# Kernel tuning notes

Hardware: AMD Instinct MI355X
Metric: run time of the kernel (lower is better)

The kernel has to match this reference:

```python
import jax, jax.numpy as jnp
import numpy as np

# Fixed production-scale dims (see shape_source)
B, R, WIDTH, T, H, W = 8, 12, 2304, 4, 16, 29
REDUCE, HID, NC, ROI_SP, DEPTH = 1024, 512, 60, 7, 2
SR = 2  # roi_align sampling ratio (fixed; torchvision default -1 is roi-adaptive)


def conv2d(x, w, pad):
    return jax.lax.conv_general_dilated(
        x, w, (1, 1), [(pad, pad), (pad, pad)],
        dimension_numbers=('NCHW', 'OIHW', 'NCHW'))


def maxpool_3x3_s2(x):
    return jax.lax.reduce_window(
        x, -jnp.inf, jax.lax.max, (1, 1, 3, 3), (1, 1, 2, 2),
        [(0, 0), (0, 0), (1, 1), (1, 1)])


def bilinear(img, ys, xs):
    # img [C,h,w]; ys, xs [P] -> [C,P]; matches torchvision bilinear_interpolate
    h, w = img.shape[1], img.shape[2]
    valid = (ys >= -1.0) & (ys <= h) & (xs >= -1.0) & (xs <= w)
    y = jnp.clip(ys, 0.0, h - 1.0)
    x = jnp.clip(xs, 0.0, w - 1.0)
    y0f = jnp.floor(y); x0f = jnp.floor(x)
    iy0 = y0f.astype(jnp.int32); ix0 = x0f.astype(jnp.int32)
    iy1 = jnp.minimum(iy0 + 1, h - 1); ix1 = jnp.minimum(ix0 + 1, w - 1)
    ly = y - y0f; lx = x - x0f; hy = 1.0 - ly; hx = 1.0 - lx
    v00 = img[:, iy0, ix0]; v01 = img[:, iy0, ix1]
    v10 = img[:, iy1, ix0]; v11 = img[:, iy1, ix1]
    out = hy * hx * v00 + hy * lx * v01 + ly * hx * v10 + ly * lx * v11
    return jnp.where(valid[None, :], out, 0.0)


def roi_align_one(img, box):
    # img [C,H,W]; box (x1,y1,x2,y2) in feature coords; aligned=False, scale=1
    x1, y1, x2, y2 = box[0], box[1], box[2], box[3]
    rw = jnp.maximum(x2 - x1, 1.0)
    rh = jnp.maximum(y2 - y1, 1.0)
    bw = rw / ROI_SP; bh = rh / ROI_SP
    g = (jnp.arange(ROI_SP, dtype=jnp.float32)[:, None]
         + (jnp.arange(SR, dtype=jnp.float32)[None, :] + 0.5) / SR).reshape(-1)  # [7*SR]
    ys = y1 + g * bh; xs = x1 + g * bw
    n = ROI_SP * SR
    yy = jnp.repeat(ys, n); xx = jnp.tile(xs, n)
    vals = bilinear(img, yy, xx)                       # [C, n*n]
    vals = vals.reshape(img.shape[0], ROI_SP, SR, ROI_SP, SR)
    return vals.mean(axis=(2, 4))                      # [C,7,7]


def hr2o_layer(x, qw, kw, vw, cw, gamma, beta):
    # x [R, HID, Hp, Wp]; non-local attention across ROIs of one image
    q = conv2d(x, qw, 1)
    k = conv2d(x, kw, 1)
    v = conv2d(x, vw, 1)
    att = jnp.einsum('ichw,jchw->ijhw', q, k) / jnp.sqrt(jnp.float32(HID))
    att = jax.nn.softmax(att, axis=1)                  # softmax over key rois
    virt = jnp.einsum('ijhw,jchw->ichw', att, v)
    mu = virt.mean(axis=(1, 2, 3), keepdims=True)      # GroupNorm(1, HID)
    var = virt.var(axis=(1, 2, 3), keepdims=True)
    virt = (virt - mu) / jnp.sqrt(var + 1e-5)
    virt = virt * gamma[None, :, None, None] + beta[None, :, None, None]
    virt = jax.nn.relu(virt)
    virt = conv2d(virt, cw, 1)                         # mlp_1x1=False -> 3x3 pad 1
    return x + virt                                    # dropout inactive in eval


def setup_inputs() -> dict:
    key = jax.random.key(0)
    ks = jax.random.split(key, 14)
    features = jax.random.normal(ks[0], (B, WIDTH, T, H, W), jnp.float32)
    xy = jax.random.uniform(ks[1], (B, R, 2), minval=0.0, maxval=0.6)
    wh = jax.random.uniform(ks[2], (B, R, 2), minval=0.2, maxval=0.4)
    rois = jnp.concatenate([xy, xy + wh], axis=-1)     # normalized x1,y1,x2,y2

    def w_(k, shape, fan_in):
        return jax.random.normal(k, shape, jnp.float32) * (1.0 / np.sqrt(fan_in))

    return {
        'features': features,
        'rois': rois,
        'conv_reduce_w': w_(ks[3], (REDUCE, WIDTH, 1, 1), WIDTH),
        'conv1_w': w_(ks[4], (HID, 2 * REDUCE, 1, 1), 2 * REDUCE),
        'conv2_w': w_(ks[5], (HID, HID, 3, 3), HID * 9),
        'hr2o_qw': w_(ks[6], (DEPTH, HID, HID, 3, 3), HID * 9),
        'hr2o_kw': w_(ks[7], (DEPTH, HID, HID, 3, 3), HID * 9),
        'hr2o_vw': w_(ks[8], (DEPTH, HID, HID, 3, 3), HID * 9),
        'hr2o_cw': w_(ks[9], (DEPTH, HID, HID, 3, 3), HID * 9),
        'hr2o_gamma': jnp.ones((DEPTH, HID), jnp.float32),
        'hr2o_beta': jnp.zeros((DEPTH, HID), jnp.float32),
        'fc1_w': w_(ks[10], (HID, REDUCE), REDUCE),
        'fc2_w': w_(ks[11], (NC, 2 * HID), 2 * HID),
    }


def reference(features, rois, conv_reduce_w, conv1_w, conv2_w,
              hr2o_qw, hr2o_kw, hr2o_vw, hr2o_cw, hr2o_gamma, hr2o_beta,
              fc1_w, fc2_w):
    feats = features.mean(axis=2)                      # AdaptiveAvgPool3d((1,H,W)) over T
    feats = conv2d(feats, conv_reduce_w, 0)            # [B, REDUCE, H, W]

    scale = jnp.array([W, H, W, H], jnp.float32)
    boxes = rois * scale                               # feature-space coords (detached)
    ra = jax.vmap(lambda img, bxs: jax.vmap(lambda b: roi_align_one(img, b))(bxs))(
        feats, boxes)                                  # [B, R, REDUCE, 7, 7]
    roi_feats = ra.max(axis=(-2, -1)).reshape(B * R, REDUCE)  # MaxPool2d(7)

    # broadcast bg + tiled actor, concat on channels (eff_h=H, eff_w=W)
    bg = jnp.broadcast_to(feats[:, None], (B, R, REDUCE, H, W))
    actor = jnp.broadcast_to(
        roi_feats.reshape(B, R, REDUCE)[..., None, None], (B, R, REDUCE, H, W))
    x = jnp.concatenate([bg, actor], axis=2).reshape(B * R, 2 * REDUCE, H, W)
    x = jax.nn.relu(conv2d(x, conv1_w, 0))             # 1x1
    x = jax.nn.relu(conv2d(x, conv2_w, 0))             # 3x3, Conv2d default pad=0
    x = maxpool_3x3_s2(x)                              # [B*R, HID, 7, 14]
    hp, wp = x.shape[2], x.shape[3]
    x = x.reshape(B, R, HID, hp, wp)
    for d in range(DEPTH):
        x = jax.vmap(lambda xi: hr2o_layer(
            xi, hr2o_qw[d], hr2o_kw[d], hr2o_vw[d], hr2o_cw[d],
            hr2o_gamma[d], hr2o_beta[d]))(x)
    high = x.mean(axis=(-2, -1)).reshape(B * R, HID)   # GAP

    out = jax.nn.relu(roi_feats @ fc1_w.T)
    out = jnp.concatenate([out, high], axis=1)
    return out @ fc2_w.T                               # [B*R, NC]
```

## Files before the change

kernel.cpp:

```cpp
#include <hip/hip_runtime.h>
#include <math.h>

#define BB 8
#define RR 12
#define WIDTH 2304
#define TT 4
#define HH 16
#define WW 29
#define HWIN (HH*WW)
#define REDUCE 1024
#define HID 512
#define NC 60
#define DEPTH 2
#define NIMG (BB*RR)
#define OH2 14
#define OW2 27
#define NSP2 (OH2*OW2)
#define PH 7
#define PW 14
#define NSP (PH*PW)
#define ATT_SCALE 0.044194173824159216f

typedef __attribute__((ext_vector_type(8))) short short8;
typedef __attribute__((ext_vector_type(4))) float floatx4;

__device__ __forceinline__ void split2(float v, unsigned short& h, unsigned short& l)
{
    union { float f; unsigned u; } c; c.f = v;
    unsigned hb = c.u & 0xffff0000u;
    h = (unsigned short)(hb >> 16);
    union { float f; unsigned u; } hc; hc.u = hb;
    float r = v - hc.f;
    union { float f; unsigned u; } rc; rc.f = r;
    unsigned ru = rc.u + 0x7fffu + ((rc.u >> 16) & 1u);
    l = (unsigned short)(ru >> 16);
}

__device__ __forceinline__ void gll16(const void* g, void* l)
{
    __builtin_amdgcn_global_load_lds((const __attribute__((address_space(1))) void*)g,
                                     (__attribute__((address_space(3))) void*)l,
                                     16, 0, 0);
}

#define MFMA3(d, ah_, al_, bh_, bl_) \
    d = __builtin_amdgcn_mfma_f32_16x16x32_bf16(ah_, bh_, d, 0, 0, 0); \
    d = __builtin_amdgcn_mfma_f32_16x16x32_bf16(ah_, bl_, d, 0, 0, 0); \
    d = __builtin_amdgcn_mfma_f32_16x16x32_bf16(al_, bh_, d, 0, 0, 0);

template<int TYPE, int NSEL, bool RELU, bool RESID, int KW, int KSTN, int MTOT, long PLSTR, int NREAL, bool ZX>
__global__ __launch_bounds__(256, 2)
void tap2_k(const int4* __restrict__ WA0, const int4* __restrict__ WA1, const int4* __restrict__ WA2,
            const ushort* __restrict__ BH, const ushort* __restrict__ BL,
            const float* __restrict__ Res,
            float* __restrict__ Y0, float* __restrict__ Y1, float* __restrict__ Y2)
{
    __shared__ int4 L[3872];
    const int tid = threadIdx.x;
    const int z  = ZX ? blockIdx.x : blockIdx.z;
    const int nb = ZX ? blockIdx.z : blockIdx.x;
    int by = blockIdx.y;

    const int4* WA = WA0; float* Y = Y0;
    if (NSEL == 3) {
        int sel = by >> 2; by &= 3;
        if (sel == 1) { WA = WA1; Y = Y1; }
        else if (sel == 2) { WA = WA2; Y = Y2; }
    }
    const int m0 = by * 128;
    const int lane = tid & 63, wv = tid >> 6;
    const int lrow = lane >> 4, lcol = lane & 15;
    constexpr long ALO = (long)KSTN * 4 * MTOT;

    int nU[2], gU[2]; long pbU[2]; bool vU[2];
#pragma unroll
    for (int it = 0; it < 2; ++it) {
        int u = tid + (it << 8);
        vU[it] = (u < 448);
        int uu = vU[it] ? u : 0;
        nU[it] = uu % 112; gU[it] = uu / 112;
        if (TYPE == 0) pbU[it] = nU[it];
        else {
            int gn = nb * 112 + nU[it];
            if (TYPE == 1) pbU[it] = (gn >> 5) * 29 + (gn & 31);
            else pbU[it] = min(gn, NREAL - 1);
        }
    }
    const ushort* BHz = BH + (size_t)z * PLSTR;
    const ushort* BLz = BL + (size_t)z * PLSTR;

    floatx4 acc[2][7];
#pragma unroll
    for (int mf = 0; mf < 2; ++mf)
#pragma unroll
        for (int nf = 0; nf < 7; ++nf) acc[mf][nf] = (floatx4){0.f, 0.f, 0.f, 0.f};

    short8 rbh[2], rbl[2];

#define STAGE_ISSUE(KST, BUF) { \
    int k8 = (KST) * 4; \
    _Pragma("unroll") \
    for (int j = 0; j < 4; ++j) { \
        int h = wv * 4 + j, p = h >> 3, g = (h >> 1) & 3, hf = h & 1; \
        gll16(WA + (p ? ALO : 0) + (long)(k8 + g) * MTOT + m0 + hf * 64 + lane, \
              L + (BUF) * 1936 + (p * 4 + g) * 129 + hf * 64); \
    } \
    int tap, ci0, shv; \
    if (TYPE == 2) { tap = 0; ci0 = (KST) << 5; shv = 0; } \
    else { tap = (KST) >> 4; ci0 = ((KST) & 15) << 5; int t3 = tap / 3; \
           shv = (TYPE == 0) ? t3 * 16 + (tap - t3 * 3) : t3 * 29 + (tap - t3 * 3); } \
    _Pragma("unroll") \
    for (int it = 0; it < 2; ++it) if (vU[it]) { \
        size_t o = (size_t)(pbU[it] + shv) * KW + ci0 + gU[it] * 8; \
        rbh[it] = *(const short8*)(BHz + o); \
        rbl[it] = *(const short8*)(BLz + o); \
    } }

#define STAGE_WRITE(BUF) { \
    _Pragma("unroll") \
    for (int it = 0; it < 2; ++it) if (vU[it]) { \
        *((short8*)(L + (BUF) * 1936 + 1032 + gU[it] * 113 + nU[it])) = rbh[it]; \
        *((short8*)(L + (BUF) * 1936 + 1484 + gU[it] * 113 + nU[it])) = rbl[it]; \
    } }

#define COMPUTE(BUF) { \
    const int4* Lc = L + (BUF) * 1936; \
    short8 ah[2], al[2]; \
    _Pragma("unroll") \
    for (int mf = 0; mf < 2; ++mf) { \
        int au = lrow * 129 + (wv * 2 + mf) * 16 + lcol; \
        ah[mf] = *(const short8*)(Lc + au); \
        al[mf] = *(const short8*)(Lc + 516 + au); \
    } \
    _Pragma("unroll") \
    for (int nf = 0; nf < 7; ++nf) { \
        int bu = 1032 + lrow * 113 + nf * 16 + lcol; \
        short8 bh = *(const short8*)(Lc + bu); \
        short8 bl = *(const short8*)(Lc + bu + 452); \
        _Pragma("unroll") \
        for (int mf = 0; mf < 2; ++mf) { MFMA3(acc[mf][nf], ah[mf], al[mf], bh, bl) } \
    } }

    STAGE_ISSUE(0, 0)
    STAGE_WRITE(0)
    __syncthreads();

    int cur = 0;
    for (int kst = 0; kst < KSTN; ++kst) {
        int nxt = cur ^ 1;
        bool more = (kst + 1 < KSTN);
        if (more) STAGE_ISSUE(kst + 1, nxt)
        COMPUTE(cur)
        if (more) { STAGE_WRITE(nxt) __syncthreads(); }
        cur = nxt;
    }

#pragma unroll
    for (int mf = 0; mf < 2; ++mf) {
        int m = m0 + wv * 32 + mf * 16 + lrow * 4;
#pragma unroll
        for (int nf = 0; nf < 7; ++nf) {
            int col = nf * 16 + lcol;
            int sp, realn; bool ok;
            if (TYPE == 0) { int oh = col >> 4, ow = col & 15; ok = ow < 14; sp = oh * 14 + ow; realn = 98; }
            else if (TYPE == 1) { int gn = nb * 112 + col; int oh = gn >> 5, ow = gn & 31; ok = ow < 27; sp = oh * 27 + ow; realn = 378; }
            else { int gn = nb * 112 + col; ok = gn < NREAL; sp = gn; realn = NREAL; }
            if (ok) {
#pragma unroll
                for (int r = 0; r < 4; ++r) {
                    size_t idx = ((size_t)z * MTOT + m + r) * realn + sp;
                    float v = acc[mf][nf][r];
                    if (RESID) v += Res[idx];
                    if (RELU) v = fmaxf(v, 0.f);
                    Y[idx] = v;
                }
            }
        }
    }
#undef STAGE_ISSUE
#undef STAGE_WRITE
#undef COMPUTE
}

__global__ void prep_w_k(const float* __restrict__ s0, const float* __restrict__ s1,
                         const float* __restrict__ s2, const float* __restrict__ s3,
                         int4* __restrict__ dst)
{
    const int c = blockIdx.y;
    const float* src = (c == 0) ? s0 : (c == 1) ? s1 : (c == 2) ? s2 : s3;
    int4* dh = dst + (size_t)c * 589824;
    int4* dl = dh + 294912;
    int idx = blockIdx.x * 256 + threadIdx.x;
    if (idx >= 294912) return;
    int g8 = idx / 512, m = idx & 511;
    unsigned hw[4], lw[4];
#pragma unroll
    for (int j = 0; j < 4; ++j) {
        int k1 = g8 * 8 + 2 * j, k2 = k1 + 1;
        float v1 = src[(size_t)m * 4608 + ((k1 & 511) * 9 + (k1 >> 9))];
        float v2 = src[(size_t)m * 4608 + ((k2 & 511) * 9 + (k2 >> 9))];
        unsigned short h0, l0, h1, l1;
        split2(v1, h0, l0); split2(v2, h1, l1);
        hw[j] = (unsigned)h0 | ((unsigned)h1 << 16);
        lw[j] = (unsigned)l0 | ((unsigned)l1 << 16);
    }
    dh[idx] = make_int4(hw[0], hw[1], hw[2], hw[3]);
    dl[idx] = make_int4(lw[0], lw[1], lw[2], lw[3]);
}

__global__ void prep_wg_k(const float* __restrict__ src, int ldw, int M, int K8,
                          int4* __restrict__ dst)
{
    int idx = blockIdx.x * 256 + threadIdx.x;
    if (idx >= K8 * M) return;
    int g8 = idx / M, m = idx % M;
    unsigned hw[4], lw[4];
#pragma unroll
    for (int j = 0; j < 4; ++j) {
        int k1 = g8 * 8 + 2 * j;
        float v1 = src[(size_t)m * ldw + k1];
        float v2 = src[(size_t)m * ldw + k1 + 1];
        unsigned short h0, l0, h1, l1;
        split2(v1, h0, l0); split2(v2, h1, l1);
        hw[j] = (unsigned)h0 | ((unsigned)h1 << 16);
        lw[j] = (unsigned)l0 | ((unsigned)l1 << 16);
    }
    dst[idx] = make_int4(hw[0], hw[1], hw[2], hw[3]);
    dst[(size_t)K8 * M + idx] = make_int4(lw[0], lw[1], lw[2], lw[3]);
}

__global__ __launch_bounds__(256)
void tsplit_k(const float* __restrict__ src, ushort* __restrict__ dh, ushort* __restrict__ dl,
              int C, int S, long zsrc, long zdst)
{
    __shared__ float t[64][65];
    const int c0 = blockIdx.x * 64, s0 = blockIdx.y * 64, z = blockIdx.z;
    const float* sz = src + (size_t)z * zsrc;
    const int tx = threadIdx.x & 63, ty = threadIdx.x >> 6;
#pragma unroll
    for (int i = 0; i < 16; ++i) {
        int cc = i * 4 + ty;
        int c = c0 + cc, s = s0 + tx;
        t[cc][tx] = (c < C && s < S) ? sz[(size_t)c * S + s] : 0.f;
    }
    __syncthreads();
#pragma unroll
    for (int i = 0; i < 16; ++i) {
        int ss = i * 4 + ty;
        int s = s0 + ss, c = c0 + tx;
        if (s < S && c < C) {
            unsigned short h, l;
            split2(t[tx][ss], h, l);
            size_t o = (size_t)z * zdst + (size_t)s * C + c;
            dh[o] = h; dl[o] = l;
        }
    }
}

__global__ __launch_bounds__(256)
void tsplit_c2_k(const float* __restrict__ bg, const float* __restrict__ bias1,
                 ushort* __restrict__ dh, ushort* __restrict__ dl)
{
    __shared__ float t[64][65];
    const int c0 = blockIdx.x * 64, s0 = blockIdx.y * 64, z = blockIdx.z;
    const int b = z / RR;
    const int tx = threadIdx.x & 63, ty = threadIdx.x >> 6;
#pragma unroll
    for (int i = 0; i < 16; ++i) {
        int cc = i * 4 + ty;
        int s = s0 + tx;
        t[cc][tx] = (s < 464) ? bg[((size_t)b * 512 + c0 + cc) * 464 + s] : 0.f;
    }
    __syncthreads();
    const float bv = bias1[z * 512 + c0 + tx];
#pragma unroll
    for (int i = 0; i < 16; ++i) {
        int ss = i * 4 + ty;
        int s = s0 + ss, c = c0 + tx;
        if (s < 472) {
            float v = (s < 464) ? fmaxf(t[tx][ss] + bv, 0.f) : 0.f;
            unsigned short h, l;
            split2(v, h, l);
            size_t o = (size_t)z * 241664 + (size_t)s * 512 + c;
            dh[o] = h; dl[o] = l;
        }
    }
}

__global__ __launch_bounds__(256)
void tsplit_pad_k(const float* __restrict__ x, ushort* __restrict__ dh, ushort* __restrict__ dl)
{
    __shared__ float t[64 * 99];
    const int c0 = blockIdx.x * 64, z = blockIdx.y;
    const int tid = threadIdx.x;
#pragma unroll
    for (int i = 0; i < 25; ++i) {
        int idx = tid + i * 256;
        if (idx < 6272) {
            int c = idx / 98, s = idx % 98;
            t[c * 99 + s] = x[((size_t)z * 512 + c0 + c) * 98 + s];
        }
    }
    __syncthreads();
#pragma unroll
    for (int i = 0; i < 40; ++i) {
        int idx = tid + i * 256;
        int sp = idx >> 6, c = idx & 63;
        int r = sp >> 4, col = sp & 15;
        float v = (r >= 1 && r <= 7 && col >= 1 && col <= 14) ? t[c * 99 + (r - 1) * 14 + col - 1] : 0.f;
        unsigned short h, l;
        split2(v, h, l);
        size_t o = (size_t)z * 81920 + (size_t)sp * 512 + c0 + c;
        dh[o] = h; dl[o] = l;
    }
}

__global__ void tmean_k(const float* __restrict__ f, float* __restrict__ o, int total)
{
    int i = blockIdx.x * blockDim.x + threadIdx.x;
    if (i >= total) return;
    int p = i % HWIN; long bc = i / HWIN;
    const float* src = f + bc * (long)TT * HWIN + p;
    o[i] = (src[0] + src[HWIN] + src[2 * HWIN] + src[3 * HWIN]) * 0.25f;
}

__global__ __launch_bounds__(256)
void roi_align_k(const float* __restrict__ feats, const float* __restrict__ rois,
                 float* __restrict__ roi_feats)
{
    __shared__ int s_o00[196], s_o01[196], s_o10[196], s_o11[196];
    __shared__ float s_w[4][196];
    const int n = blockIdx.x;
    const int b = n / RR;
    const int t = threadIdx.x;
    if (t < 196) {
        float x1 = rois[n * 4 + 0] * WW, y1 = rois[n * 4 + 1] * HH;
        float x2 = rois[n * 4 + 2] * WW, y2 = rois[n * 4 + 3] * HH;
        float rw = fmaxf(x2 - x1, 1.f), rh = fmaxf(y2 - y1, 1.f);
        float bw = rw / 7.f, bh = rh / 7.f;
        int j = t / 14, i = t % 14;
        float gy = (float)(j >> 1) + ((j & 1) + 0.5f) * 0.5f;
        float gx = (float)(i >> 1) + ((i & 1) + 0.5f) * 0.5f;
        float ys = y1 + gy * bh, xs = x1 + gx * bw;
        bool valid = (ys >= -1.f) && (ys <= (float)HH) && (xs >= -1.f) && (xs <= (float)WW);
        float y = fminf(fmaxf(ys, 0.f), (float)(HH - 1));
        float x = fminf(fmaxf(xs, 0.f), (float)(WW - 1));
        float y0f = floorf(y), x0f = floorf(x);
        int iy0 = (int)y0f, ix0 = (int)x0f;
        int iy1 = min(iy0 + 1, HH - 1), ix1 = min(ix0 + 1, WW - 1);
        float ly = y - y0f, lx = x - x0f, hy = 1.f - ly, hx = 1.f - lx;
        float msk = valid ? 1.f : 0.f;
        s_o00[t] = iy0 * WW + ix0; s_o01[t] = iy0 * WW + ix1;
        s_o10[t] = iy1 * WW + ix0; s_o11[t] = iy1 * WW + ix1;
        s_w[0][t] = hy * hx * msk; s_w[1][t] = hy * lx * msk;
        s_w[2][t] = ly * hx * msk; s_w[3][t] = ly * lx * msk;
    }
    __syncthreads();
    for (int c = t; c < REDUCE; c += 256) {
        const float* img = feats + ((long)(b * REDUCE + c)) * HWIN;
        float mx = -INFINITY;
        for (int bin = 0; bin < 49; ++bin) {
            int by_ = bin / 7, bx = bin % 7;
            float s = 0.f;
#pragma unroll
            for (int sy = 0; sy < 2; ++sy)
#pragma unroll
                for (int sx = 0; sx < 2; ++sx) {
                    int ss = (by_ * 2 + sy) * 14 + bx * 2 + sx;
                    s += s_w[0][ss] * img[s_o00[ss]] + s_w[1][ss] * img[s_o01[ss]]
                       + s_w[2][ss] * img[s_o10[ss]] + s_w[3][ss] * img[s_o11[ss]];
                }
            mx = fmaxf(mx, s * 0.25f);
        }
        roi_feats[(long)n * REDUCE + c] = mx;
    }
}

__global__ void dots_k(const float* __restrict__ Xr, const float* __restrict__ Wt,
                       int ldw, int woff, float* __restrict__ Y,
                       int Nrows, int M, int K, int relu)
{
    int idx = blockIdx.x * blockDim.x + threadIdx.x;
    if (idx >= Nrows * M) return;
    int o = idx / Nrows, n = idx % Nrows;
    const float* xr = Xr + (long)n * K;
    const float* w = Wt + (long)o * ldw + woff;
    float acc = 0.f;
    for (int k = 0; k < K; ++k) acc = fmaf(xr[k], w[k], acc);
    if (relu) acc = fmaxf(acc, 0.f);
    Y[(long)n * M + o] = acc;
}

__global__ void maxpool_k(const float* __restrict__ in, float* __restrict__ out, int total)
{
    int idx = blockIdx.x * blockDim.x + threadIdx.x;
    if (idx >= total) return;
    int ow = idx % PW; int r = idx / PW; int oh = r % PH; long nc = r / PH;
    const float* src = in + nc * NSP2;
    float m = -INFINITY;
    for (int kh = 0; kh < 3; ++kh) {
        int ih = oh * 2 - 1 + kh; if (ih < 0 || ih >= OH2) continue;
        for (int kw = 0; kw < 3; ++kw) {
            int iw = ow * 2 - 1 + kw; if (iw < 0 || iw >= OW2) continue;
            m = fmaxf(m, src[ih * OW2 + iw]);
        }
    }
    out[idx] = m;
}

__global__ __launch_bounds__(256)
void att2_k(const float* __restrict__ q, const float* __restrict__ k, float* __restrict__ att)
{
    __shared__ float qs[5376];
    __shared__ float ks[5376];
    __shared__ float sc[1008];
    const int b = blockIdx.x, p0 = blockIdx.y * 7;
    const int tid = threadIdx.x;

    int itI[4], itJ[4], itP[4]; bool itV[4];
#pragma unroll
    for (int r = 0; r < 4; ++r) {
        int item = tid + (r << 8);
        itV[r] = item < 1008;
        int it = itV[r] ? item : 0;
        int ij = it / 7; itP[r] = it % 7;
        itI[r] = ij / 12; itJ[r] = ij % 12;
    }
    float acc[4] = {0.f, 0.f, 0.f, 0.f};

    for (int cc0 = 0; cc0 < 512; cc0 += 64) {
        for (int l = tid; l < 5376; l += 256) {
            int i = l / 448, r = l % 448, c = r / 7, p = r % 7;
            size_t off = ((size_t)(b * 12 + i) * 512 + cc0 + c) * 98 + p0 + p;
            qs[l] = q[off];
            ks[l] = k[off];
        }
        __syncthreads();
#pragma unroll
        for (int r = 0; r < 4; ++r) {
            if (itV[r]) {
                const float* qp = qs + itI[r] * 448 + itP[r];
                const float* kp = ks + itJ[r] * 448 + itP[r];
                float a = acc[r];
#pragma unroll 8
                for (int c = 0; c < 64; ++c) a = fmaf(qp[c * 7], kp[c * 7], a);
                acc[r] = a;
            }
        }
        __syncthreads();
    }
#pragma unroll
    for (int r = 0; r < 4; ++r)
        if (itV[r]) sc[tid + (r << 8)] = acc[r] * ATT_SCALE;
    __syncthreads();
    if (tid < 84) {
        int i = tid / 7, p = tid % 7;
        float m = -INFINITY;
        float v[12];
#pragma unroll
        for (int j = 0; j < 12; ++j) { v[j] = sc[(i * 12 + j) * 7 + p]; m = fmaxf(m, v[j]); }
        float s = 0.f;
#pragma unroll
        for (int j = 0; j < 12; ++j) { v[j] = expf(v[j] - m); s += v[j]; }
        float inv = 1.f / s;
#pragma unroll
        for (int j = 0; j < 12; ++j)
            att[((size_t)(b * 12 + i) * 12 + j) * 98 + p0 + p] = v[j] * inv;
    }
}

__global__ __launch_bounds__(256)
void virt2_k(const float* __restrict__ att, const float* __restrict__ v, float* __restrict__ virt)
{
    __shared__ float as_[14112];
    const int b = blockIdx.x, cb = blockIdx.y;
    const int tid = threadIdx.x;
    for (int l = tid; l < 14112; l += 256) as_[l] = att[(size_t)b * 14112 + l];
    __syncthreads();

    for (int it = tid; it < 6272; it += 256) {
        int c = cb * 64 + it / 98, p = it % 98;
        float o[12];
#pragma unroll
        for (int i = 0; i < 12; ++i) o[i] = 0.f;
#pragma unroll
        for (int j = 0; j < 12; ++j) {
            float vj = v[((size_t)(b * 12 + j) * 512 + c) * 98 + p];
#pragma unroll
            for (int i = 0; i < 12; ++i) o[i] = fmaf(as_[(i * 12 + j) * 98 + p], vj, o[i]);
        }
#pragma unroll
        for (int i = 0; i < 12; ++i)
            virt[((size_t)(b * 12 + i) * 512 + c) * 98 + p] = o[i];
    }
}

__global__ __launch_bounds__(256)
void stats_k(const float* __restrict__ virt, float* __restrict__ mu, float* __restrict__ rstd)
{
    int n = blockIdx.x;
    const float* src = virt + (long)n * HID * NSP;
    float s = 0.f, q = 0.f;
    for (int i = threadIdx.x; i < HID * NSP; i += 256) {
        float v = src[i]; s += v; q = fmaf(v, v, q);
    }
    for (int off = 32; off; off >>= 1) { s += __shfl_down(s, off); q += __shfl_down(q, off); }
    __shared__ float ss[4], sq[4];
    int w = threadIdx.x >> 6;
    if ((threadIdx.x & 63) == 0) { ss[w] = s; sq[w] = q; }
    __syncthreads();
    if (threadIdx.x == 0) {
        float S = ss[0] + ss[1] + ss[2] + ss[3];
        float Q = sq[0] + sq[1] + sq[2] + sq[3];
        const float invN = 1.f / (HID * NSP);
        float m = S * invN;
        float var = Q * invN - m * m;
        mu[n] = m; rstd[n] = rsqrtf(var + 1e-5f);
    }
}

__global__ void norm_k(float* __restrict__ virt, const float* __restrict__ mu,
                       const float* __restrict__ rstd,
                       const float* __restrict__ gamma, const float* __restrict__ beta)
{
    int idx = blockIdx.x * blockDim.x + threadIdx.x;
    const int TOT = NIMG * HID * NSP;
    if (idx >= TOT) return;
    int n = idx / (HID * NSP);
    int c = (idx / NSP) % HID;
    float val = (virt[idx] - mu[n]) * rstd[n] * gamma[c] + beta[c];
    virt[idx] = fmaxf(val, 0.f);
}

__global__ void meanpool_k(const float* __restrict__ x, float* __restrict__ high)
{
    int idx = blockIdx.x * blockDim.x + threadIdx.x;
    if (idx >= NIMG * HID) return;
    const float* src = x + (long)idx * NSP;
    float s = 0.f;
    for (int p = 0; p < NSP; ++p) s += src[p];
    high[idx] = s * (1.f / NSP);
}

__global__ void final_k(const float* __restrict__ fc1o, const float* __restrict__ high,
                        const float* __restrict__ fc2, float* __restrict__ out)
{
    int idx = blockIdx.x * blockDim.x + threadIdx.x;
    if (idx >= NIMG * NC) return;
    int n = idx / NC, o = idx % NC;
    const float* w = fc2 + (long)o * (2 * HID);
    const float* a = fc1o + (long)n * HID;
    const float* h = high + (long)n * HID;
    float acc = 0.f;
    for (int c = 0; c < HID; ++c) acc = fmaf(a[c], w[c], acc);
    for (int c = 0; c < HID; ++c) acc = fmaf(h[c], w[HID + c], acc);
    out[idx] = acc;
}

extern "C" void kernel_launch(void* const* d_in, const int* in_sizes, int n_in,
                              void* d_out, int out_size, void* d_ws, size_t ws_size,
                              hipStream_t stream)
{
    (void)in_sizes; (void)n_in; (void)out_size; (void)ws_size;
    const float* features = (const float*)d_in[0];
    const float* rois     = (const float*)d_in[1];
    const float* w_reduce = (const float*)d_in[2];
    const float* w_conv1  = (const float*)d_in[3];
    const float* w_conv2  = (const float*)d_in[4];
    const float* qw       = (const float*)d_in[5];
    const float* kw       = (const float*)d_in[6];
    const float* vw       = (const float*)d_in[7];
    const float* cw       = (const float*)d_in[8];
    const float* gamma    = (const float*)d_in[9];
    const float* beta     = (const float*)d_in[10];
    const float* fc1      = (const float*)d_in[11];
    const float* fc2      = (const float*)d_in[12];
    float* ws = (float*)d_ws;

    float*  tmean = ws + 0;
    ushort* tmTH  = (ushort*)(ws + 8552448);
    ushort* tmTL  = (ushort*)(ws + 12828672);
    float*  feats = ws + 17104896;
    ushort* ftTH  = (ushort*)(ws + 0);
    ushort* ftTL  = (ushort*)(ws + 1900544);
    ushort* B2H   = (ushort*)(ws + 0);
    ushort* B2L   = (ushort*)(ws + 11599872);
    int4*   WTQ   = (int4*)(ws + 0);
    float*  bg    = ws + 23199744;
    float*  out2  = ws + 23199744;
    float*  qb    = ws + 23199744;
    float*  kb    = ws + 28016640;
    float*  vb    = ws + 32833536;
    ushort* PTH   = (ushort*)(ws + 41779200);
    ushort* PTL   = (ushort*)(ws + 45711360);
    float*  xb    = ws + 49643520;
    float*  virt  = ws + 54460416;
    int4*   WTS   = (int4*)(ws + 59277312);
    float*  rf    = ws + 61636608;
    float*  bias1 = ws + 61734912;
    float*  fc1o  = ws + 61784064;
    float*  attb  = ws + 61833216;
    float*  mu    = ws + 61946112;
    float*  rstd  = ws + 61946240;
    float*  high  = ws + 61946368;

    dim3 blk(256);

    prep_wg_k<<<1152, blk, 0, stream>>>(w_reduce, 2304, 1024, 288, WTS);

    { int tot = BB * WIDTH * HWIN;
      tmean_k<<<(tot + 255) / 256, blk, 0, stream>>>(features, tmean, tot); }

    tsplit_k<<<dim3(36, 8, 8), blk, 0, stream>>>(tmean, tmTH, tmTL, 2304, 464, 1069056, 1069056);

    tap2_k<2, 1, false, false, 2304, 72, 1024, 464L * 2304, 464, false>
        <<<dim3(5, 8, 8), blk, 0, stream>>>(WTS, nullptr, nullptr, tmTH, tmTL, nullptr,
                                            feats, nullptr, nullptr);

    tsplit_k<<<dim3(16, 8, 8), blk, 0, stream>>>(feats, ftTH, ftTL, 1024, 464, 475136, 475136);

    roi_align_k<<<96, blk, 0, stream>>>(feats, rois, rf);
    dots_k<<<(NIMG * HID + 255) / 256, blk, 0, stream>>>(rf, w_conv1, 2048, 1024, bias1, NIMG, HID, REDUCE, 0);
    dots_k<<<(NIMG * HID + 255) / 256, blk, 0, stream>>>(rf, fc1, 1024, 0, fc1o, NIMG, HID, REDUCE, 1);

    prep_wg_k<<<256, blk, 0, stream>>>(w_conv1, 2048, 512, 128, WTS);
    tap2_k<2, 1, false, false, 1024, 32, 512, 464L * 1024, 464, false>
        <<<dim3(5, 4, 8), blk, 0, stream>>>(WTS, nullptr, nullptr, ftTH, ftTL, nullptr,
                                            bg, nullptr, nullptr);

    prep_w_k<<<dim3(1152, 1), blk, 0, stream>>>(w_conv2, w_conv2, w_conv2, w_conv2, WTS);
    tsplit_c2_k<<<dim3(8, 8, 96), blk, 0, stream>>>(bg, bias1, B2H, B2L);

    tap2_k<1, 1, true, false, 512, 144, 512, 472L * 512, 378, true>
        <<<dim3(96, 4, 4), blk, 0, stream>>>(WTS, nullptr, nullptr, B2H, B2L, nullptr,
                                             out2, nullptr, nullptr);

    { int tot = NIMG * HID * NSP;
      maxpool_k<<<(tot + 255) / 256, blk, 0, stream>>>(out2, xb, tot); }

    for (int d = 0; d < DEPTH; ++d) {
        long woff = (long)d * HID * HID * 9;
        prep_w_k<<<dim3(1152, 4), blk, 0, stream>>>(qw + woff, kw + woff, vw + woff, cw + woff, WTQ);

        tsplit_pad_k<<<dim3(8, 96), blk, 0, stream>>>(xb, PTH, PTL);
        tap2_k<0, 3, false, false, 512, 144, 512, 160L * 512, 98, true>
            <<<dim3(96, 12, 1), blk, 0, stream>>>(WTQ, WTQ + 589824, WTQ + 2 * 589824,
                                                  PTH, PTL, nullptr, qb, kb, vb);

        att2_k<<<dim3(8, 14), blk, 0, stream>>>(qb, kb, attb);
        virt2_k<<<dim3(8, 8), blk, 0, stream>>>(attb, vb, virt);
        stats_k<<<96, blk, 0, stream>>>(virt, mu, rstd);
        { int tot = NIMG * HID * NSP;
          norm_k<<<(tot + 255) / 256, blk, 0, stream>>>(virt, mu, rstd, gamma + d * HID, beta + d * HID); }

        tsplit_pad_k<<<dim3(8, 96), blk, 0, stream>>>(virt, PTH, PTL);
        tap2_k<0, 1, false, true, 512, 144, 512, 160L * 512, 98, true>
            <<<dim3(96, 4, 1), blk, 0, stream>>>(WTQ + 3 * 589824, nullptr, nullptr,
                                                 PTH, PTL, xb, xb, nullptr, nullptr);
    }

    meanpool_k<<<(NIMG * HID + 255) / 256, blk, 0, stream>>>(xb, high);
    final_k<<<(NIMG * NC + 255) / 256, blk, 0, stream>>>(fc1o, high, fc2, (float*)d_out);
}
```

Baseline: 3.314 ms.

## Add larger-tile 3x3 conv GEMM kernel with 512 threads and remapped block order

Adds a new tap3_k kernel for the 3x3 convolutions (conv2, QKV and output convs) that uses 512-thread blocks with 256x224 output tiles. Two images or a wider spatial slab share each weight tile, so weight loads are reused more and per-block overhead drops. The kernel uses a custom block-index swizzle for cache locality and dynamic LDS of about 124KB. The old tap2_k is trimmed to serve only the 1x1 GEMMs. The trade-off is more registers (28 accumulators per thread), fewer blocks, and possibly lower occupancy or a tail effect, e.g. only 96 blocks for the output conv.

```diff
diff --git a/kernel.cpp b/kernel.cpp
--- a/kernel.cpp
+++ b/kernel.cpp
@@ -48,25 +48,172 @@
     d = __builtin_amdgcn_mfma_f32_16x16x32_bf16(ah_, bl_, d, 0, 0, 0); \
     d = __builtin_amdgcn_mfma_f32_16x16x32_bf16(al_, bh_, d, 0, 0, 0);
 
-template<int TYPE, int NSEL, bool RELU, bool RESID, int KW, int KSTN, int MTOT, long PLSTR, int NREAL, bool ZX>
-__global__ __launch_bounds__(256, 2)
-void tap2_k(const int4* __restrict__ WA0, const int4* __restrict__ WA1, const int4* __restrict__ WA2,
+template<int GEOM, int NSEL, bool RELU, bool RESID>
+__global__ __launch_bounds__(512, 2)
+void tap3_k(const int4* __restrict__ WA0, const int4* __restrict__ WA1, const int4* __restrict__ WA2,
             const ushort* __restrict__ BH, const ushort* __restrict__ BL,
             const float* __restrict__ Res,
             float* __restrict__ Y0, float* __restrict__ Y1, float* __restrict__ Y2)
 {
+    extern __shared__ int4 L[];
+    const int tid = threadIdx.x;
+    const int bid = blockIdx.x;
+    int m0, z0, z1 = 0, nb = 0, sel = 0;
+    if (GEOM == 0) {
+        int s = bid & 7, r = bid >> 3;
+        int zq = s & 3, yq = s >> 2;
+        int y = yq * 3 + r % 3;
+        int zp = zq * 12 + r / 3;
+        sel = y >> 1; m0 = (y & 1) * 256;
+        z0 = zp * 2; z1 = z0 + 1;
+    } else if (GEOM == 1) {
+        int s = bid & 7, r = bid >> 3;
+        m0 = (s & 1) * 256;
+        nb = r & 1; z0 = (s >> 1) * 24 + (r >> 1); z1 = z0;
+    } else {
+        int s = bid & 7, r = bid >> 3;
+        m0 = (s & 1) * 256;
+        int zp = (s >> 1) * 12 + r;
+        z0 = zp * 2; z1 = z0 + 1;
+    }
+    const int4* WA = (NSEL == 3) ? (sel == 0 ? WA0 : sel == 1 ? WA1 : WA2) : WA0;
+    float* Y = (NSEL == 3) ? (sel == 0 ? Y0 : sel == 1 ? Y1 : Y2) : Y0;
+
+    const int lane = tid & 63, wv = tid >> 6;
+    const int lrow = lane >> 4, lcol = lane & 15;
+    constexpr long ALO = 294912;
+    constexpr long PLSTR = (GEOM == 1) ? 472L * 512 : 160L * 512;
+
+    const long abase = ((wv >> 2) ? ALO : 0) + m0;
+    const int ag = wv & 3;
+
+    int nU[2], gU[2]; bool vU[2];
+    const ushort* bhp[2]; const ushort* blp[2];
+#pragma unroll
+    for (int it = 0; it < 2; ++it) {
+        int u = tid + (it << 9);
+        vU[it] = (u < 896);
+        int uu = vU[it] ? u : 0;
+        nU[it] = uu % 224; gU[it] = uu / 224;
+        long pb; int zsel;
+        if (GEOM == 1) {
+            int gn = nb * 224 + nU[it];
+            pb = (gn >> 5) * 29 + (gn & 31); zsel = z0;
+        } else {
+            int hi = nU[it] >= 112;
+            pb = nU[it] - (hi ? 112 : 0); zsel = hi ? z1 : z0;
+        }
+        bhp[it] = BH + (size_t)zsel * PLSTR + pb * 512 + gU[it] * 8;
+        blp[it] = BL + (size_t)zsel * PLSTR + pb * 512 + gU[it] * 8;
+    }
+
+    floatx4 acc[2][14];
+#pragma unroll
+    for (int mf = 0; mf < 2; ++mf)
+#pragma unroll
+        for (int nf = 0; nf < 14; ++nf) acc[mf][nf] = (floatx4){0.f, 0.f, 0.f, 0.f};
+
+    short8 rbh[2], rbl[2];
+
+#define STAGE_ISSUE(KST, BUF) { \
+    int k8 = (KST) * 4; \
+    _Pragma("unroll") \
+    for (int j = 0; j < 4; ++j) \
+        gll16(WA + abase + (long)(k8 + ag) * 512 + j * 64 + lane, \
+              L + (BUF) * 2064 + wv * 258 + j * 64); \
+    int tap = (KST) >> 4, ci0 = ((KST) & 15) << 5; \
+    int t3 = tap / 3; \
+    int boff = ((GEOM == 1) ? (t3 * 29 + tap - t3 * 3) : (t3 * 16 + tap - t3 * 3)) * 512 + ci0; \
+    _Pragma("unroll") \
+    for (int it = 0; it < 2; ++it) if (vU[it]) { \
+        rbh[it] = *(const short8*)(bhp[it] + boff); \
+        rbl[it] = *(const short8*)(blp[it] + boff); \
+    } }
+
+#define STAGE_WRITE(BUF) { \
+    _Pragma("unroll") \
+    for (int it = 0; it < 2; ++it) if (vU[it]) { \
+        *((short8*)(L + 4128 + (BUF) * 1800 + gU[it] * 225 + nU[it])) = rbh[it]; \
+        *((short8*)(L + 4128 + (BUF) * 1800 + 900 + gU[it] * 225 + nU[it])) = rbl[it]; \
+    } }
+
+#define COMPUTE(BUF) { \
+    const int4* La = L + (BUF) * 2064; \
+    const int4* Lb = L + 4128 + (BUF) * 1800; \
+    short8 ah[2], al[2]; \
+    _Pragma("unroll") \
+    for (int mf = 0; mf < 2; ++mf) { \
+        int au = lrow * 258 + (wv * 2 + mf) * 16 + lcol; \
+        ah[mf] = *(const short8*)(La + au); \
+        al[mf] = *(const short8*)(La + 1032 + au); \
+    } \
+    _Pragma("unroll") \
+    for (int nf = 0; nf < 14; ++nf) { \
+        int bu = lrow * 225 + nf * 16 + lcol; \
+        short8 bh = *(const short8*)(Lb + bu); \
+        short8 bl = *(const short8*)(Lb + 900 + bu); \
+        _Pragma("unroll") \
+        for (int mf = 0; mf < 2; ++mf) { MFMA3(acc[mf][nf], ah[mf], al[mf], bh, bl) } \
+    } }
+
+    STAGE_ISSUE(0, 0)
+    STAGE_WRITE(0)
+    __syncthreads();
+
+    int cur = 0;
+    for (int kst = 0; kst < 144; ++kst) {
+        int nxt = cur ^ 1;
+        bool more = (kst + 1 < 144);
+        if (more) STAGE_ISSUE(kst + 1, nxt)
+        COMPUTE(cur)
+        if (more) { STAGE_WRITE(nxt) __syncthreads(); }
+        cur = nxt;
+    }
+
+#pragma unroll
+    for (int mf = 0; mf < 2; ++mf) {
+        int m = m0 + wv * 32 + mf * 16 + lrow * 4;
+#pragma unroll
+        for (int nf = 0; nf < 14; ++nf) {
+            int col = nf * 16 + lcol;
+            int sp, realn, z; bool ok;
+            if (GEOM == 1) {
+                int gn = nb * 224 + col;
+                int oh = gn >> 5, ow = gn & 31;
+                ok = ow < 27; sp = oh * 27 + ow; realn = 378; z = z0;
+            } else {
+                int cm = col - (nf >= 7 ? 112 : 0);
+                int oh = cm >> 4, ow = cm & 15;
+                ok = ow < 14; sp = oh * 14 + ow; realn = 98;
+                z = (nf >= 7) ? z1 : z0;
+            }
+            if (ok) {
+#pragma unroll
+                for (int r = 0; r < 4; ++r) {
+                    size_t idx = ((size_t)z * 512 + m + r) * realn + sp;
+                    float v = acc[mf][nf][r];
+                    if (RESID) v += Res[idx];
+                    if (RELU) v = fmaxf(v, 0.f);
+                    Y[idx] = v;
+                }
+            }
+        }
+    }
+#undef STAGE_ISSUE
+#undef STAGE_WRITE
+#undef COMPUTE
+}
+
+template<int KW, int KSTN, int MTOT, long PLSTR, int NREAL>
+__global__ __launch_bounds__(256, 2)
+void tap2_k(const int4* __restrict__ WA,
+            const ushort* __restrict__ BH, const ushort* __restrict__ BL,
+            float* __restrict__ Y)
+{
     __shared__ int4 L[3872];
     const int tid = threadIdx.x;
-    const int z  = ZX ? blockIdx.x : blockIdx.z;
-    const int nb = ZX ? blockIdx.z : blockIdx.x;
-    int by = blockIdx.y;
-
-    const int4* WA = WA0; float* Y = Y0;
-    if (NSEL == 3) {
-        int sel = by >> 2; by &= 3;
-        if (sel == 1) { WA = WA1; Y = Y1; }
-        else if (sel == 2) { WA = WA2; Y = Y2; }
-    }
+    const int z = blockIdx.z, nb = blockIdx.x;
+    const int by = blockIdx.y;
     const int m0 = by * 128;
     const int lane = tid & 63, wv = tid >> 6;
     const int lrow = lane >> 4, lcol = lane & 15;
@@ -79,12 +226,8 @@
         vU[it] = (u < 448);
         int uu = vU[it] ? u : 0;
         nU[it] = uu % 112; gU[it] = uu / 112;
-        if (TYPE == 0) pbU[it] = nU[it];
-        else {
-            int gn = nb * 112 + nU[it];
-            if (TYPE == 1) pbU[it] = (gn >> 5) * 29 + (gn & 31);
-            else pbU[it] = min(gn, NREAL - 1);
-        }
+        int gn = nb * 112 + nU[it];
+        pbU[it] = min(gn, NREAL - 1);
     }
     const ushort* BHz = BH + (size_t)z * PLSTR;
     const ushort* BLz = BL + (size_t)z * PLSTR;
@@ -105,13 +248,10 @@
         gll16(WA + (p ? ALO : 0) + (long)(k8 + g) * MTOT + m0 + hf * 64 + lane, \
               L + (BUF) * 1936 + (p * 4 + g) * 129 + hf * 64); \
     } \
-    int tap, ci0, shv; \
-    if (TYPE == 2) { tap = 0; ci0 = (KST) << 5; shv = 0; } \
-    else { tap = (KST) >> 4; ci0 = ((KST) & 15) << 5; int t3 = tap / 3; \
-           shv = (TYPE == 0) ? t3 * 16 + (tap - t3 * 3) : t3 * 29 + (tap - t3 * 3); } \
+    int ci0 = (KST) << 5; \
     _Pragma("unroll") \
     for (int it = 0; it < 2; ++it) if (vU[it]) { \
-        size_t o = (size_t)(pbU[it] + shv) * KW + ci0 + gU[it] * 8; \
+        size_t o = (size_t)pbU[it] * KW + ci0 + gU[it] * 8; \
         rbh[it] = *(const short8*)(BHz + o); \
         rbl[it] = *(const short8*)(BLz + o); \
     } }
@@ -161,18 +301,12 @@
 #pragma unroll
         for (int nf = 0; nf < 7; ++nf) {
             int col = nf * 16 + lcol;
-            int sp, realn; bool ok;
-            if (TYPE == 0) { int oh = col >> 4, ow = col & 15; ok = ow < 14; sp = oh * 14 + ow; realn = 98; }
-            else if (TYPE == 1) { int gn = nb * 112 + col; int oh = gn >> 5, ow = gn & 31; ok = ow < 27; sp = oh * 27 + ow; realn = 378; }
-            else { int gn = nb * 112 + col; ok = gn < NREAL; sp = gn; realn = NREAL; }
-            if (ok) {
+            int gn = nb * 112 + col;
+            if (gn < NREAL) {
 #pragma unroll
                 for (int r = 0; r < 4; ++r) {
-                    size_t idx = ((size_t)z * MTOT + m + r) * realn + sp;
-                    float v = acc[mf][nf][r];
-                    if (RESID) v += Res[idx];
-                    if (RELU) v = fmaxf(v, 0.f);
-                    Y[idx] = v;
+                    size_t idx = ((size_t)z * MTOT + m + r) * NREAL + gn;
+                    Y[idx] = acc[mf][nf][r];
                 }
             }
         }
@@ -605,6 +739,7 @@
     float*  high  = ws + 61946368;
 
     dim3 blk(256);
+    const size_t BIG_LDS = 7728 * sizeof(int4);
 
     prep_wg_k<<<1152, blk, 0, stream>>>(w_reduce, 2304, 1024, 288, WTS);
 
@@ -613,9 +748,8 @@
 
     tsplit_k<<<dim3(36, 8, 8), blk, 0, stream>>>(tmean, tmTH, tmTL, 2304, 464, 1069056, 1069056);
 
-    tap2_k<2, 1, false, false, 2304, 72, 1024, 464L * 2304, 464, false>
-        <<<dim3(5, 8, 8), blk, 0, stream>>>(WTS, nullptr, nullptr, tmTH, tmTL, nullptr,
-                                            feats, nullptr, nullptr);
+    tap2_k<2304, 72, 1024, 464L * 2304, 464>
+        <<<dim3(5, 8, 8), blk, 0, stream>>>(WTS, tmTH, tmTL, feats);
 
     tsplit_k<<<dim3(16, 8, 8), blk, 0, stream>>>(feats, ftTH, ftTL, 1024, 464, 475136, 475136);
 
@@ -624,16 +758,14 @@
     dots_k<<<(NIMG * HID + 255) / 256, blk, 0, stream>>>(rf, fc1, 1024, 0, fc1o, NIMG, HID, REDUCE, 1);
 
     prep_wg_k<<<256, blk, 0, stream>>>(w_conv1, 2048, 512, 128, WTS);
-    tap2_k<2, 1, false, false, 1024, 32, 512, 464L * 1024, 464, false>
-        <<<dim3(5, 4, 8), blk, 0, stream>>>(WTS, nullptr, nullptr, ftTH, ftTL, nullptr,
-                                            bg, nullptr, nullptr);
+    tap2_k<1024, 32, 512, 464L * 1024, 464>
+        <<<dim3(5, 4, 8), blk, 0, stream>>>(WTS, ftTH, ftTL, bg);
 
     prep_w_k<<<dim3(1152, 1), blk, 0, stream>>>(w_conv2, w_conv2, w_conv2, w_conv2, WTS);
     tsplit_c2_k<<<dim3(8, 8, 96), blk, 0, stream>>>(bg, bias1, B2H, B2L);
 
-    tap2_k<1, 1, true, false, 512, 144, 512, 472L * 512, 378, true>
-        <<<dim3(96, 4, 4), blk, 0, stream>>>(WTS, nullptr, nullptr, B2H, B2L, nullptr,
-                                             out2, nullptr, nullptr);
+    tap3_k<1, 1, true, false><<<384, 512, BIG_LDS, stream>>>(
+        WTS, nullptr, nullptr, B2H, B2L, nullptr, out2, nullptr, nullptr);
 
     { int tot = NIMG * HID * NSP;
       maxpool_k<<<(tot + 255) / 256, blk, 0, stream>>>(out2, xb, tot); }
@@ -643,9 +775,8 @@
         prep_w_k<<<dim3(1152, 4), blk, 0, stream>>>(qw + woff, kw + woff, vw + woff, cw + woff, WTQ);
 
         tsplit_pad_k<<<dim3(8, 96), blk, 0, stream>>>(xb, PTH, PTL);
-        tap2_k<0, 3, false, false, 512, 144, 512, 160L * 512, 98, true>
-            <<<dim3(96, 12, 1), blk, 0, stream>>>(WTQ, WTQ + 589824, WTQ + 2 * 589824,
-                                                  PTH, PTL, nullptr, qb, kb, vb);
+        tap3_k<0, 3, false, false><<<288, 512, BIG_LDS, stream>>>(
+            WTQ, WTQ + 589824, WTQ + 2 * 589824, PTH, PTL, nullptr, qb, kb, vb);
 
         att2_k<<<dim3(8, 14), blk, 0, stream>>>(qb, kb, attb);
         virt2_k<<<dim3(8, 8), blk, 0, stream>>>(attb, vb, virt);
@@ -654,9 +785,8 @@
           norm_k<<<(tot + 255) / 256, blk, 0, stream>>>(virt, mu, rstd, gamma + d * HID, beta + d * HID); }
 
         tsplit_pad_k<<<dim3(8, 96), blk, 0, stream>>>(virt, PTH, PTL);
-        tap2_k<0, 1, false, true, 512, 144, 512, 160L * 512, 98, true>
-            <<<dim3(96, 4, 1), blk, 0, stream>>>(WTQ + 3 * 589824, nullptr, nullptr,
-                                                 PTH, PTL, xb, xb, nullptr, nullptr);
+        tap3_k<2, 1, false, true><<<96, 512, BIG_LDS, stream>>>(
+            WTQ + 3 * 589824, nullptr, nullptr, PTH, PTL, xb, xb, nullptr, nullptr);
     }
 
     meanpool_k<<<(NIMG * HID + 255) / 256, blk, 0, stream>>>(xb, high);
```

Result: slower. 4.082 ms (+23.2%).

## Reuse staged input rows across all nine 3x3 taps and two images per block

Applied to the files above, without the earlier changes.

The 3x3 convolutions get a new kernel that copies one 32-channel block of the padded input rows for two images into shared memory once, then runs all nine taps from it by shifting the LDS read offset. Before, the input was re-read from global for every tap. The weight reorder in prep_w_k is changed to match a channel-block-major, tap-minor K order. Each block now computes two images, which doubles the accumulator count and raises register pressure, and the grids get fewer, larger blocks. 1x1 convolutions move to a separate simplified kernel.

```diff
diff --git a/kernel.cpp b/kernel.cpp
--- a/kernel.cpp
+++ b/kernel.cpp
@@ -48,26 +48,163 @@
     d = __builtin_amdgcn_mfma_f32_16x16x32_bf16(ah_, bl_, d, 0, 0, 0); \
     d = __builtin_amdgcn_mfma_f32_16x16x32_bf16(al_, bh_, d, 0, 0, 0);
 
-template<int TYPE, int NSEL, bool RELU, bool RESID, int KW, int KSTN, int MTOT, long PLSTR, int NREAL, bool ZX>
+template<int TYPE, int NSEL, bool RELU, bool RESID, int WR>
 __global__ __launch_bounds__(256, 2)
-void tap2_k(const int4* __restrict__ WA0, const int4* __restrict__ WA1, const int4* __restrict__ WA2,
+void tapr_k(const int4* __restrict__ WA0, const int4* __restrict__ WA1, const int4* __restrict__ WA2,
             const ushort* __restrict__ BH, const ushort* __restrict__ BL,
             const float* __restrict__ Res,
             float* __restrict__ Y0, float* __restrict__ Y1, float* __restrict__ Y2)
 {
+    __shared__ int4 L[2064 + 16 * WR];
+    const int tid = threadIdx.x;
+
+    int ch, zp, nb = 0;
+    if (TYPE == 0) { ch = blockIdx.x / 48; zp = blockIdx.x % 48; }
+    else { ch = blockIdx.x / 192; int r = blockIdx.x % 192; nb = r / 48; zp = r % 48; }
+    int sel = 0, m0;
+    if (NSEL == 3) { sel = ch >> 2; m0 = (ch & 3) * 128; }
+    else m0 = ch * 128;
+    const int z0 = zp * 2;
+
+    const int4* WA = (NSEL == 3) ? (sel == 0 ? WA0 : sel == 1 ? WA1 : WA2) : WA0;
+    float* Y = (NSEL == 3) ? (sel == 0 ? Y0 : sel == 1 ? Y1 : Y2) : Y0;
+
+    const int lane = tid & 63, wv = tid >> 6;
+    const int lrow = lane >> 4, lcol = lane & 15;
+    constexpr long ALO = 294912;
+    constexpr long PLSTR = (TYPE == 1) ? 472L * 512 : 160L * 512;
+    const int pbase = (TYPE == 1) ? (((nb * 112) >> 5) * 29 + ((nb * 112) & 31)) : 0;
+
+    int pbnf[7];
+#pragma unroll
+    for (int nf = 0; nf < 7; ++nf) {
+        int col = nf * 16 + lcol;
+        if (TYPE == 0) pbnf[nf] = col;
+        else { int gn = nb * 112 + col; pbnf[nf] = (gn >> 5) * 29 + (gn & 31) - pbase; }
+    }
+
+    int uR[3], uPl[3], uZi[3]; bool uV[3];
+    const ushort* uSrc[3];
+#pragma unroll
+    for (int it = 0; it < 3; ++it) {
+        int u = tid + it * 256;
+        uV[it] = (u < 4 * WR);
+        int uu = uV[it] ? u : 0;
+        uR[it] = uu % WR; uPl[it] = (uu / WR) & 1; uZi[it] = uu / (2 * WR);
+        const ushort* P = uPl[it] ? BL : BH;
+        uSrc[it] = P + (size_t)(z0 + uZi[it]) * PLSTR + (size_t)(pbase + uR[it]) * 512;
+    }
+
+    floatx4 acc[2][2][7];
+#pragma unroll
+    for (int zi = 0; zi < 2; ++zi)
+#pragma unroll
+        for (int mf = 0; mf < 2; ++mf)
+#pragma unroll
+            for (int nf = 0; nf < 7; ++nf) acc[zi][mf][nf] = (floatx4){0.f, 0.f, 0.f, 0.f};
+
+#define BCOPY(CB) { \
+    _Pragma("unroll") \
+    for (int it = 0; it < 3; ++it) if (uV[it]) { \
+        const int4* s = (const int4*)(uSrc[it] + (size_t)(CB) * 32); \
+        int4 t0 = s[0], t1 = s[1], t2 = s[2], t3_ = s[3]; \
+        int bse = 2064 + uZi[it] * (8 * WR) + uPl[it] * (4 * WR) + uR[it]; \
+        L[bse] = t0; L[bse + WR] = t1; L[bse + 2 * WR] = t2; L[bse + 3 * WR] = t3_; \
+    } }
+
+#define ASTAGE(KST, BUF) { \
+    int k8 = (KST) * 4; \
+    _Pragma("unroll") \
+    for (int j = 0; j < 4; ++j) { \
+        int h = wv * 4 + j, p = h >> 3, g = (h >> 1) & 3, hf = h & 1; \
+        gll16(WA + (p ? ALO : 0) + (long)(k8 + g) * 512 + m0 + hf * 64 + lane, \
+              L + (BUF) * 1032 + (p * 4 + g) * 129 + hf * 64); \
+    } }
+
+#define COMPUTE(BUF, SHV) { \
+    const int4* La = L + (BUF) * 1032; \
+    short8 ah[2], al[2]; \
+    _Pragma("unroll") \
+    for (int mf = 0; mf < 2; ++mf) { \
+        int au = lrow * 129 + (wv * 2 + mf) * 16 + lcol; \
+        ah[mf] = *(const short8*)(La + au); \
+        al[mf] = *(const short8*)(La + 516 + au); \
+    } \
+    _Pragma("unroll") \
+    for (int nf = 0; nf < 7; ++nf) { \
+        int spl = pbnf[nf] + (SHV); \
+        _Pragma("unroll") \
+        for (int zi = 0; zi < 2; ++zi) { \
+            const int4* Lb = L + 2064 + zi * (8 * WR) + lrow * WR + spl; \
+            short8 bh = *(const short8*)(Lb); \
+            short8 bl = *(const short8*)(Lb + 4 * WR); \
+            _Pragma("unroll") \
+            for (int mf = 0; mf < 2; ++mf) { MFMA3(acc[zi][mf][nf], ah[mf], al[mf], bh, bl) } \
+        } \
+    } }
+
+    BCOPY(0)
+    ASTAGE(0, 0)
+    __syncthreads();
+
+    int cur = 0;
+    for (int cb = 0; cb < 16; ++cb) {
+#pragma unroll
+        for (int tap = 0; tap < 9; ++tap) {
+            const int kst = cb * 9 + tap;
+            const int t3 = tap / 3;
+            const int shv = (TYPE == 0) ? (t3 * 16 + (tap - t3 * 3)) : (t3 * 29 + (tap - t3 * 3));
+            if (kst < 143) ASTAGE(kst + 1, cur ^ 1)
+            COMPUTE(cur, shv)
+            __syncthreads();
+            cur ^= 1;
+        }
+        if (cb < 15) {
+            BCOPY(cb + 1)
+            __syncthreads();
+        }
+    }
+
+#pragma unroll
+    for (int zi = 0; zi < 2; ++zi) {
+        const int z = z0 + zi;
+#pragma unroll
+        for (int mf = 0; mf < 2; ++mf) {
+            int m = m0 + wv * 32 + mf * 16 + lrow * 4;
+#pragma unroll
+            for (int nf = 0; nf < 7; ++nf) {
+                int col = nf * 16 + lcol;
+                int sp, realn; bool ok;
+                if (TYPE == 0) { int oh = col >> 4, ow = col & 15; ok = ow < 14; sp = oh * 14 + ow; realn = 98; }
+                else { int gn = nb * 112 + col; int oh = gn >> 5, ow = gn & 31; ok = ow < 27; sp = oh * 27 + ow; realn = 378; }
+                if (ok) {
+#pragma unroll
+                    for (int r = 0; r < 4; ++r) {
+                        size_t idx = ((size_t)z * 512 + m + r) * realn + sp;
+                        float v = acc[zi][mf][nf][r];
+                        if (RESID) v += Res[idx];
+                        if (RELU) v = fmaxf(v, 0.f);
+                        Y[idx] = v;
+                    }
+                }
+            }
+        }
+    }
+#undef BCOPY
+#undef ASTAGE
+#undef COMPUTE
+}
+
+template<int KW, int KSTN, int MTOT, long PLSTR, int NREAL>
+__global__ __launch_bounds__(256, 2)
+void tapc_k(const int4* __restrict__ WA,
+            const ushort* __restrict__ BH, const ushort* __restrict__ BL,
+            float* __restrict__ Y)
+{
     __shared__ int4 L[3872];
     const int tid = threadIdx.x;
-    const int z  = ZX ? blockIdx.x : blockIdx.z;
-    const int nb = ZX ? blockIdx.z : blockIdx.x;
-    int by = blockIdx.y;
-
-    const int4* WA = WA0; float* Y = Y0;
-    if (NSEL == 3) {
-        int sel = by >> 2; by &= 3;
-        if (sel == 1) { WA = WA1; Y = Y1; }
-        else if (sel == 2) { WA = WA2; Y = Y2; }
-    }
-    const int m0 = by * 128;
+    const int z = blockIdx.z, nb = blockIdx.x;
+    const int m0 = blockIdx.y * 128;
     const int lane = tid & 63, wv = tid >> 6;
     const int lrow = lane >> 4, lcol = lane & 15;
     constexpr long ALO = (long)KSTN * 4 * MTOT;
@@ -79,12 +216,8 @@
         vU[it] = (u < 448);
         int uu = vU[it] ? u : 0;
         nU[it] = uu % 112; gU[it] = uu / 112;
-        if (TYPE == 0) pbU[it] = nU[it];
-        else {
-            int gn = nb * 112 + nU[it];
-            if (TYPE == 1) pbU[it] = (gn >> 5) * 29 + (gn & 31);
-            else pbU[it] = min(gn, NREAL - 1);
-        }
+        int gn = nb * 112 + nU[it];
+        pbU[it] = min(gn, NREAL - 1);
     }
     const ushort* BHz = BH + (size_t)z * PLSTR;
     const ushort* BLz = BL + (size_t)z * PLSTR;
@@ -105,13 +238,10 @@
         gll16(WA + (p ? ALO : 0) + (long)(k8 + g) * MTOT + m0 + hf * 64 + lane, \
               L + (BUF) * 1936 + (p * 4 + g) * 129 + hf * 64); \
     } \
-    int tap, ci0, shv; \
-    if (TYPE == 2) { tap = 0; ci0 = (KST) << 5; shv = 0; } \
-    else { tap = (KST) >> 4; ci0 = ((KST) & 15) << 5; int t3 = tap / 3; \
-           shv = (TYPE == 0) ? t3 * 16 + (tap - t3 * 3) : t3 * 29 + (tap - t3 * 3); } \
+    int ci0 = (KST) << 5; \
     _Pragma("unroll") \
     for (int it = 0; it < 2; ++it) if (vU[it]) { \
-        size_t o = (size_t)(pbU[it] + shv) * KW + ci0 + gU[it] * 8; \
+        size_t o = (size_t)pbU[it] * KW + ci0 + gU[it] * 8; \
         rbh[it] = *(const short8*)(BHz + o); \
         rbl[it] = *(const short8*)(BLz + o); \
     } }
@@ -161,18 +291,12 @@
 #pragma unroll
         for (int nf = 0; nf < 7; ++nf) {
             int col = nf * 16 + lcol;
-            int sp, realn; bool ok;
-            if (TYPE == 0) { int oh = col >> 4, ow = col & 15; ok = ow < 14; sp = oh * 14 + ow; realn = 98; }
-            else if (TYPE == 1) { int gn = nb * 112 + col; int oh = gn >> 5, ow = gn & 31; ok = ow < 27; sp = oh * 27 + ow; realn = 378; }
-            else { int gn = nb * 112 + col; ok = gn < NREAL; sp = gn; realn = NREAL; }
-            if (ok) {
+            int gn = nb * 112 + col;
+            if (gn < NREAL) {
 #pragma unroll
                 for (int r = 0; r < 4; ++r) {
-                    size_t idx = ((size_t)z * MTOT + m + r) * realn + sp;
-                    float v = acc[mf][nf][r];
-                    if (RESID) v += Res[idx];
-                    if (RELU) v = fmaxf(v, 0.f);
-                    Y[idx] = v;
+                    size_t idx = ((size_t)z * MTOT + m + r) * NREAL + gn;
+                    Y[idx] = acc[mf][nf][r];
                 }
             }
         }
@@ -197,8 +321,10 @@
 #pragma unroll
     for (int j = 0; j < 4; ++j) {
         int k1 = g8 * 8 + 2 * j, k2 = k1 + 1;
-        float v1 = src[(size_t)m * 4608 + ((k1 & 511) * 9 + (k1 >> 9))];
-        float v2 = src[(size_t)m * 4608 + ((k2 & 511) * 9 + (k2 >> 9))];
+        int cb1 = k1 / 288, r1 = k1 % 288, tp1 = r1 >> 5, ci1 = cb1 * 32 + (r1 & 31);
+        int cb2 = k2 / 288, r2 = k2 % 288, tp2 = r2 >> 5, ci2 = cb2 * 32 + (r2 & 31);
+        float v1 = src[(size_t)m * 4608 + ci1 * 9 + tp1];
+        float v2 = src[(size_t)m * 4608 + ci2 * 9 + tp2];
         unsigned short h0, l0, h1, l1;
         split2(v1, h0, l0); split2(v2, h1, l1);
         hw[j] = (unsigned)h0 | ((unsigned)h1 << 16);
@@ -613,9 +739,8 @@
 
     tsplit_k<<<dim3(36, 8, 8), blk, 0, stream>>>(tmean, tmTH, tmTL, 2304, 464, 1069056, 1069056);
 
-    tap2_k<2, 1, false, false, 2304, 72, 1024, 464L * 2304, 464, false>
-        <<<dim3(5, 8, 8), blk, 0, stream>>>(WTS, nullptr, nullptr, tmTH, tmTL, nullptr,
-                                            feats, nullptr, nullptr);
+    tapc_k<2304, 72, 1024, 464L * 2304, 464>
+        <<<dim3(5, 8, 8), blk, 0, stream>>>(WTS, tmTH, tmTL, feats);
 
     tsplit_k<<<dim3(16, 8, 8), blk, 0, stream>>>(feats, ftTH, ftTL, 1024, 464, 475136, 475136);
 
@@ -624,16 +749,14 @@
     dots_k<<<(NIMG * HID + 255) / 256, blk, 0, stream>>>(rf, fc1, 1024, 0, fc1o, NIMG, HID, REDUCE, 1);
 
     prep_wg_k<<<256, blk, 0, stream>>>(w_conv1, 2048, 512, 128, WTS);
-    tap2_k<2, 1, false, false, 1024, 32, 512, 464L * 1024, 464, false>
-        <<<dim3(5, 4, 8), blk, 0, stream>>>(WTS, nullptr, nullptr, ftTH, ftTL, nullptr,
-                                            bg, nullptr, nullptr);
+    tapc_k<1024, 32, 512, 464L * 1024, 464>
+        <<<dim3(5, 4, 8), blk, 0, stream>>>(WTS, ftTH, ftTL, bg);
 
     prep_w_k<<<dim3(1152, 1), blk, 0, stream>>>(w_conv2, w_conv2, w_conv2, w_conv2, WTS);
     tsplit_c2_k<<<dim3(8, 8, 96), blk, 0, stream>>>(bg, bias1, B2H, B2L);
 
-    tap2_k<1, 1, true, false, 512, 144, 512, 472L * 512, 378, true>
-        <<<dim3(96, 4, 4), blk, 0, stream>>>(WTS, nullptr, nullptr, B2H, B2L, nullptr,
-                                             out2, nullptr, nullptr);
+    tapr_k<1, 1, true, false, 164><<<768, blk, 0, stream>>>(
+        WTS, nullptr, nullptr, B2H, B2L, nullptr, out2, nullptr, nullptr);
 
     { int tot = NIMG * HID * NSP;
       maxpool_k<<<(tot + 255) / 256, blk, 0, stream>>>(out2, xb, tot); }
@@ -643,9 +766,8 @@
         prep_w_k<<<dim3(1152, 4), blk, 0, stream>>>(qw + woff, kw + woff, vw + woff, cw + woff, WTQ);
 
         tsplit_pad_k<<<dim3(8, 96), blk, 0, stream>>>(xb, PTH, PTL);
-        tap2_k<0, 3, false, false, 512, 144, 512, 160L * 512, 98, true>
-            <<<dim3(96, 12, 1), blk, 0, stream>>>(WTQ, WTQ + 589824, WTQ + 2 * 589824,
-                                                  PTH, PTL, nullptr, qb, kb, vb);
+        tapr_k<0, 3, false, false, 160><<<576, blk, 0, stream>>>(
+            WTQ, WTQ + 589824, WTQ + 2 * 589824, PTH, PTL, nullptr, qb, kb, vb);
 
         att2_k<<<dim3(8, 14), blk, 0, stream>>>(qb, kb, attb);
         virt2_k<<<dim3(8, 8), blk, 0, stream>>>(attb, vb, virt);
@@ -654,9 +776,8 @@
           norm_k<<<(tot + 255) / 256, blk, 0, stream>>>(virt, mu, rstd, gamma + d * HID, beta + d * HID); }
 
         tsplit_pad_k<<<dim3(8, 96), blk, 0, stream>>>(virt, PTH, PTL);
-        tap2_k<0, 1, false, true, 512, 144, 512, 160L * 512, 98, true>
-            <<<dim3(96, 4, 1), blk, 0, stream>>>(WTQ + 3 * 589824, nullptr, nullptr,
-                                                 PTH, PTL, xb, xb, nullptr, nullptr);
+        tapr_k<0, 1, false, true, 160><<<192, blk, 0, stream>>>(
+            WTQ + 3 * 589824, nullptr, nullptr, PTH, PTL, xb, xb, nullptr, nullptr);
     }
 
     meanpool_k<<<(NIMG * HID + 255) / 256, blk, 0, stream>>>(xb, high);
```

Result: faster. 2.971 ms (-10.3%).
